# Kernel tuning notes

Hardware: AMD Instinct MI355X
Metric: run time of the kernel (lower is better)

Reference implementation:

```python
import jax, jax.numpy as jnp
import numpy as np

PERTURBATION_SCALE = 0.01

def setup_inputs() -> dict:
    key = jax.random.key(0)
    k1, k2, k3 = jax.random.split(key, 3)
    theta = jax.random.normal(k1, (256, 512), dtype=jnp.float32)
    basis_eval = jax.random.normal(k2, (100000, 512), dtype=jnp.float32)
    noise = jax.random.normal(k3, (256, 512), dtype=jnp.float32)
    return {"theta": theta, "basis_eval": basis_eval, "noise": noise}

def reference(theta, basis_eval, noise):
    # phi: [N, K] functional evaluations
    phi_raw = basis_eval @ theta.T
    phi_perturbed = basis_eval @ (theta + noise * PERTURBATION_SCALE).T
    # sign-crossings between consecutive evaluation points: [N-1, K]
    crossings = (phi_raw[:-1] * phi_raw[1:] < 0).astype(theta.dtype)
    crossings_p = (phi_perturbed[:-1] * phi_perturbed[1:] < 0).astype(theta.dtype)
    persistence = crossings * crossings_p  # [N-1, K]
    # fused pairwise shared-persistence: Gram matrix [K, K]
    gram = persistence.T @ persistence
    K = theta.shape[0]
    iu, ju = jnp.triu_indices(K, k=1)  # row-major i<j == itertools.combinations order
    return gram[iu, ju]  # [K*(K-1)/2]
```

## Files before the change

### kernel.cpp

```cpp
#include <hip/hip_runtime.h>
#include <hip/hip_bf16.h>
#include <stdint.h>

#define KDIM    256
#define NWORDS  1564
#define NW      1563

typedef float  f32x4  __attribute__((ext_vector_type(4)));
typedef __bf16 bf16x8 __attribute__((ext_vector_type(8)));
typedef __bf16 bf16x4 __attribute__((ext_vector_type(4)));

__global__ void build_w(const float* __restrict__ theta,
                        const float* __restrict__ noise,
                        __bf16* __restrict__ Wt) {
    int idx = blockIdx.x * 256 + threadIdx.x;
    int j = idx >> 9;
    int d = idx & 511;
    float v;
    if (j < KDIM) v = theta[j * 512 + d];
    else          v = theta[(j - KDIM) * 512 + d] + 0.01f * noise[(j - KDIM) * 512 + d];
    Wt[((d >> 5) * 512 + j) * 32 + (d & 31)] = (__bf16)v;
}

__global__ void __launch_bounds__(512, 4)
gemm_signs(const float* __restrict__ basis,
           const __bf16* __restrict__ Wt,
           uint64_t* __restrict__ sbits) {
    __shared__ char smem[34816];

    const int tid    = threadIdx.x;
    const int lane   = tid & 63;
    const int wc     = tid >> 6;
    const int lane16 = lane & 15;
    const int lgrp   = lane >> 4;

    const int orig = blockIdx.x;
    const int x    = orig & 7;
    const int bm   = (x < 4 ? x * 196 : 784 + (x - 4) * 195) + (orig >> 3);

    const int rl  = tid >> 3;
    const int oct = tid & 7;
    int r = bm * 64 + rl; if (r > 99999) r = 99999;
    const float* asrc = basis + (size_t)r * 512 + oct * 4;
    const int awofs = rl * 64 + (((oct >> 1) ^ ((rl >> 1) & 3)) << 4) + ((oct & 1) << 3);

    const char* wbase = (const char*)Wt;
    int bfofs[4];
    #pragma unroll
    for (int n = 0; n < 4; ++n)
        bfofs[n] = (wc * 64 + n * 16 + lane16) * 64 + lgrp * 16;

    f32x4  acc[4][4] = {};
    float4 ra[2];
    bf16x8 bf[2][4];

    ra[0] = *(const float4*)(asrc);
    ra[1] = *(const float4*)(asrc + 32);
    #pragma unroll
    for (int n = 0; n < 4; ++n)
        bf[0][n] = *(const bf16x8*)(wbase + bfofs[n]);
    {
        bf16x4 v;
        v[0] = (__bf16)ra[0].x; v[1] = (__bf16)ra[0].y;
        v[2] = (__bf16)ra[0].z; v[3] = (__bf16)ra[0].w;
        *(bf16x4*)(smem + awofs) = v;
    }
    asm volatile("s_waitcnt lgkmcnt(0)" ::: "memory");

    #pragma unroll
    for (int t = 0; t < 16; ++t) {
        if (t < 14) ra[t & 1] = *(const float4*)(asrc + (t + 2) * 32);
        if (t < 15) {
            #pragma unroll
            for (int n = 0; n < 4; ++n)
                bf[(t + 1) & 1][n] =
                    *(const bf16x8*)(wbase + (size_t)(t + 1) * 32768 + bfofs[n]);
        }

        __builtin_amdgcn_s_barrier();

        if (t < 15) {
            bf16x4 v;
            float4 rv = ra[(t + 1) & 1];
            v[0] = (__bf16)rv.x; v[1] = (__bf16)rv.y;
            v[2] = (__bf16)rv.z; v[3] = (__bf16)rv.w;
            *(bf16x4*)(smem + (((t + 1) & 1) << 12) + awofs) = v;
        }

        const char* ab = smem + ((t & 1) << 12);
        #pragma unroll
        for (int mh = 0; mh < 2; ++mh) {
            bf16x8 af[2];
            #pragma unroll
            for (int mi = 0; mi < 2; ++mi) {
                int rr = (mh * 2 + mi) * 16 + lane16;
                af[mi] = *(const bf16x8*)(ab + rr * 64
                           + ((lgrp ^ ((rr >> 1) & 3)) << 4));
            }
            asm volatile("s_waitcnt lgkmcnt(0)" ::: "memory");
            __builtin_amdgcn_sched_barrier(0);
            __builtin_amdgcn_s_setprio(1);
            #pragma unroll
            for (int mi = 0; mi < 2; ++mi)
                #pragma unroll
                for (int n = 0; n < 4; ++n)
                    acc[mh * 2 + mi][n] = __builtin_amdgcn_mfma_f32_16x16x32_bf16(
                        af[mi], bf[t & 1][n], acc[mh * 2 + mi][n], 0, 0, 0);
            __builtin_amdgcn_s_setprio(0);
        }
    }

    __builtin_amdgcn_s_barrier();
    unsigned char* sb = (unsigned char*)smem;
    #pragma unroll
    for (int m = 0; m < 4; ++m) {
        #pragma unroll
        for (int n = 0; n < 4; ++n) {
            int cc = wc * 64 + n * 16 + lane16;
            int rb = m * 16 + lgrp * 4;
            uint32_t pk = 0;
            #pragma unroll
            for (int rg = 0; rg < 4; ++rg)
                pk |= (acc[m][n][rg] < 0.0f ? 1u : 0u) << (8 * rg);
            *(uint32_t*)&sb[cc * 68 + rb] = pk;
        }
    }
    asm volatile("s_waitcnt lgkmcnt(0)" ::: "memory");
    __builtin_amdgcn_s_barrier();

    {
        const unsigned char* src = &sb[tid * 68];
        uint64_t wbits = 0;
        #pragma unroll
        for (int k = 0; k < 16; ++k) {
            uint32_t qv = *(const uint32_t*)&src[4 * k];
            uint32_t p4 = ((qv & 0x01010101u) * 0x10204080u) >> 28;
            wbits |= (uint64_t)p4 << (4 * k);
        }
        sbits[(size_t)bm * 512 + tid] = wbits;
    }
}

__global__ void crossing_masks(const uint64_t* __restrict__ sbits,
                               uint64_t* __restrict__ maskT) {
    const int w = blockIdx.x;
    const int j = threadIdx.x;
    uint64_t s0r = sbits[(size_t)w * 512 + j];
    uint64_t s0p = sbits[(size_t)w * 512 + 256 + j];
    uint64_t s1r = sbits[(size_t)(w + 1) * 512 + j];
    uint64_t s1p = sbits[(size_t)(w + 1) * 512 + 256 + j];
    uint64_t cr = s0r ^ ((s0r >> 1) | (s1r << 63));
    uint64_t cp = s0p ^ ((s0p >> 1) | (s1p << 63));
    uint64_t m = cr & cp;
    if (w == NW - 1) m &= 0x7FFFFFFFull;
    maskT[(size_t)w * 256 + j] = m;
}

__global__ void zero_out(float* __restrict__ out) {
    int i = blockIdx.x * 256 + threadIdx.x;
    if (i < 32640) out[i] = 0.0f;
}

__global__ void pair_popcount(const uint64_t* __restrict__ maskT,
                              float* __restrict__ out) {
    const int i = blockIdx.x;
    const int c = blockIdx.y;
    const int j = threadIdx.x;
    if (j <= i) return;
    int w0 = c * 196;
    int w1 = w0 + 196; if (w1 > NW) w1 = NW;
    uint32_t sum = 0;
    #pragma unroll 4
    for (int w = w0; w < w1; ++w) {
        uint64_t mi = maskT[(size_t)w * 256 + i];
        uint64_t mj = maskT[(size_t)w * 256 + j];
        sum += (uint32_t)__popcll(mi & mj);
    }
    const size_t idx = (size_t)i * (2 * KDIM - i - 1) / 2 + (size_t)(j - i - 1);
    atomicAdd(&out[idx], (float)sum);
}

extern "C" void kernel_launch(void* const* d_in, const int* in_sizes, int n_in,
                              void* d_out, int out_size, void* d_ws, size_t ws_size,
                              hipStream_t stream) {
    const float* theta = (const float*)d_in[0];
    const float* basis = (const float*)d_in[1];
    const float* noise = (const float*)d_in[2];
    float* out = (float*)d_out;

    char* ws = (char*)d_ws;
    __bf16*   Wt    = (__bf16*)ws;
    uint64_t* sbits = (uint64_t*)(ws + 524288);
    uint64_t* maskT = (uint64_t*)(ws + 524288 + (size_t)NWORDS * 512 * 8);

    hipLaunchKernelGGL(build_w,        dim3(1024),    dim3(256), 0, stream, theta, noise, Wt);
    hipLaunchKernelGGL(gemm_signs,     dim3(NWORDS),  dim3(512), 0, stream, basis, Wt, sbits);
    hipLaunchKernelGGL(crossing_masks, dim3(NW),      dim3(256), 0, stream, sbits, maskT);
    hipLaunchKernelGGL(zero_out,       dim3(128),     dim3(256), 0, stream, out);
    hipLaunchKernelGGL(pair_popcount,  dim3(KDIM, 8), dim3(256), 0, stream, maskT, out);
}
```

Baseline: 122.5 us.

## Stage A tiles in 128-wide K chunks to cut barriers in GEMM loop

The A-operand staging in gemm_signs is restructured to load 128 K-elements per row per stage into a larger double-buffered LDS region with XOR swizzling over 16 slots. This drops block barriers from one per 32-K step to one per 128-K step and loads all four A fragments before issuing 16 MFMAs. It also removes the explicit per-half lgkmcnt wait. Launch bounds drop to 2 blocks per CU, which permits more registers for the larger prefetch state but risks lower occupancy.

```diff
diff --git a/kernel.cpp b/kernel.cpp
--- a/kernel.cpp
+++ b/kernel.cpp
@@ -8,7 +8,6 @@
 
 typedef float  f32x4  __attribute__((ext_vector_type(4)));
 typedef __bf16 bf16x8 __attribute__((ext_vector_type(8)));
-typedef __bf16 bf16x4 __attribute__((ext_vector_type(4)));
 
 __global__ void build_w(const float* __restrict__ theta,
                         const float* __restrict__ noise,
@@ -22,7 +21,7 @@
     Wt[((d >> 5) * 512 + j) * 32 + (d & 31)] = (__bf16)v;
 }
 
-__global__ void __launch_bounds__(512, 4)
+__global__ void __launch_bounds__(512, 2)
 gemm_signs(const float* __restrict__ basis,
            const __bf16* __restrict__ Wt,
            uint64_t* __restrict__ sbits) {
@@ -41,8 +40,8 @@
     const int rl  = tid >> 3;
     const int oct = tid & 7;
     int r = bm * 64 + rl; if (r > 99999) r = 99999;
-    const float* asrc = basis + (size_t)r * 512 + oct * 4;
-    const int awofs = rl * 64 + (((oct >> 1) ^ ((rl >> 1) & 3)) << 4) + ((oct & 1) << 3);
+    const float* ag = basis + (size_t)r * 512 + oct * 16;
+    const int gsz = rl & 15;
 
     const char* wbase = (const char*)Wt;
     int bfofs[4];
@@ -51,62 +50,70 @@
         bfofs[n] = (wc * 64 + n * 16 + lane16) * 64 + lgrp * 16;
 
     f32x4  acc[4][4] = {};
-    float4 ra[2];
-    bf16x8 bf[2][4];
-
-    ra[0] = *(const float4*)(asrc);
-    ra[1] = *(const float4*)(asrc + 32);
-    #pragma unroll
-    for (int n = 0; n < 4; ++n)
-        bf[0][n] = *(const bf16x8*)(wbase + bfofs[n]);
-    {
-        bf16x4 v;
-        v[0] = (__bf16)ra[0].x; v[1] = (__bf16)ra[0].y;
-        v[2] = (__bf16)ra[0].z; v[3] = (__bf16)ra[0].w;
-        *(bf16x4*)(smem + awofs) = v;
-    }
+    float4 ra[4];
+    bf16x8 bfr[2][4];
+
+    auto write_A = [&](int q) {
+        char* wb = smem + (q << 14);
+        #pragma unroll
+        for (int u = 0; u < 2; ++u) {
+            bf16x8 w;
+            w[0] = (__bf16)ra[2*u].x;   w[1] = (__bf16)ra[2*u].y;
+            w[2] = (__bf16)ra[2*u].z;   w[3] = (__bf16)ra[2*u].w;
+            w[4] = (__bf16)ra[2*u+1].x; w[5] = (__bf16)ra[2*u+1].y;
+            w[6] = (__bf16)ra[2*u+1].z; w[7] = (__bf16)ra[2*u+1].w;
+            *(bf16x8*)(wb + rl * 256 + (((2*oct + u) ^ gsz) << 4)) = w;
+        }
+    };
+
+    #pragma unroll
+    for (int u = 0; u < 4; ++u) ra[u] = *(const float4*)(ag + u * 4);
+    #pragma unroll
+    for (int n = 0; n < 4; ++n) bfr[0][n] = *(const bf16x8*)(wbase + bfofs[n]);
+    write_A(0);
+    #pragma unroll
+    for (int u = 0; u < 4; ++u) ra[u] = *(const float4*)(ag + 128 + u * 4);
     asm volatile("s_waitcnt lgkmcnt(0)" ::: "memory");
-
-    #pragma unroll
-    for (int t = 0; t < 16; ++t) {
-        if (t < 14) ra[t & 1] = *(const float4*)(asrc + (t + 2) * 32);
-        if (t < 15) {
+    __builtin_amdgcn_s_barrier();
+
+    #pragma unroll
+    for (int s = 0; s < 4; ++s) {
+        const char* ab = smem + ((s & 1) << 14);
+        #pragma unroll
+        for (int ti = 0; ti < 4; ++ti) {
+            const int t = s * 4 + ti;
+            if (t < 15) {
+                #pragma unroll
+                for (int n = 0; n < 4; ++n)
+                    bfr[(t + 1) & 1][n] =
+                        *(const bf16x8*)(wbase + (size_t)(t + 1) * 32768 + bfofs[n]);
+            }
+            bf16x8 af[4];
             #pragma unroll
-            for (int n = 0; n < 4; ++n)
-                bf[(t + 1) & 1][n] =
-                    *(const bf16x8*)(wbase + (size_t)(t + 1) * 32768 + bfofs[n]);
-        }
-
-        __builtin_amdgcn_s_barrier();
-
-        if (t < 15) {
-            bf16x4 v;
-            float4 rv = ra[(t + 1) & 1];
-            v[0] = (__bf16)rv.x; v[1] = (__bf16)rv.y;
-            v[2] = (__bf16)rv.z; v[3] = (__bf16)rv.w;
-            *(bf16x4*)(smem + (((t + 1) & 1) << 12) + awofs) = v;
-        }
-
-        const char* ab = smem + ((t & 1) << 12);
-        #pragma unroll
-        for (int mh = 0; mh < 2; ++mh) {
-            bf16x8 af[2];
-            #pragma unroll
-            for (int mi = 0; mi < 2; ++mi) {
-                int rr = (mh * 2 + mi) * 16 + lane16;
-                af[mi] = *(const bf16x8*)(ab + rr * 64
-                           + ((lgrp ^ ((rr >> 1) & 3)) << 4));
+            for (int m = 0; m < 4; ++m) {
+                int rr = m * 16 + lane16;
+                af[m] = *(const bf16x8*)(ab + rr * 256
+                           + (((ti * 4 + lgrp) ^ (rr & 15)) << 4));
             }
-            asm volatile("s_waitcnt lgkmcnt(0)" ::: "memory");
             __builtin_amdgcn_sched_barrier(0);
             __builtin_amdgcn_s_setprio(1);
             #pragma unroll
-            for (int mi = 0; mi < 2; ++mi)
+            for (int m = 0; m < 4; ++m)
                 #pragma unroll
                 for (int n = 0; n < 4; ++n)
-                    acc[mh * 2 + mi][n] = __builtin_amdgcn_mfma_f32_16x16x32_bf16(
-                        af[mi], bf[t & 1][n], acc[mh * 2 + mi][n], 0, 0, 0);
+                    acc[m][n] = __builtin_amdgcn_mfma_f32_16x16x32_bf16(
+                        af[m], bfr[t & 1][n], acc[m][n], 0, 0, 0);
             __builtin_amdgcn_s_setprio(0);
+        }
+        if (s < 3) {
+            write_A((s + 1) & 1);
+            if (s < 2) {
+                #pragma unroll
+                for (int u = 0; u < 4; ++u)
+                    ra[u] = *(const float4*)(ag + (s + 2) * 128 + u * 4);
+            }
+            asm volatile("s_waitcnt lgkmcnt(0)" ::: "memory");
+            __builtin_amdgcn_s_barrier();
         }
     }
 
```

Result: slower. 139.6 us (+14.0%).

## Warp-specialize GEMM into producer wave loading A and consumer MFMA waves

Applied to the files above, without the earlier changes.

Splits the sign GEMM block into 8 consumer waves doing MFMA and 2 producer waves that load basis rows, convert them to bf16 and fill a 4-slot LDS ring. Handoff uses workgroup-scope atomic ready/done counters instead of block-wide barriers each k-step. The aim is to overlap global loads with MFMA work and drop per-iteration barriers. In exchange, spin-wait polling adds overhead, and the larger block plus launch bounds may reduce occupancy and raise register pressure.

```diff
diff --git a/kernel.cpp b/kernel.cpp
--- a/kernel.cpp
+++ b/kernel.cpp
@@ -22,114 +22,152 @@
     Wt[((d >> 5) * 512 + j) * 32 + (d & 31)] = (__bf16)v;
 }
 
-__global__ void __launch_bounds__(512, 4)
-gemm_signs(const float* __restrict__ basis,
-           const __bf16* __restrict__ Wt,
-           uint64_t* __restrict__ sbits) {
-    __shared__ char smem[34816];
+__global__ void __launch_bounds__(640)
+gemm_signs_pc(const float* __restrict__ basis,
+              const __bf16* __restrict__ Wt,
+              uint64_t* __restrict__ sbits) {
+    __shared__ char smem[34848];
 
     const int tid    = threadIdx.x;
     const int lane   = tid & 63;
-    const int wc     = tid >> 6;
+    const int wave   = tid >> 6;
     const int lane16 = lane & 15;
     const int lgrp   = lane >> 4;
+
+    unsigned* ready     = (unsigned*)(smem + 34816);
+    unsigned* cons_done = (unsigned*)(smem + 34816 + 16);
+    if (tid < 8) ((unsigned*)(smem + 34816))[tid] = 0;
+    __syncthreads();
 
     const int orig = blockIdx.x;
     const int x    = orig & 7;
     const int bm   = (x < 4 ? x * 196 : 784 + (x - 4) * 195) + (orig >> 3);
 
-    const int rl  = tid >> 3;
-    const int oct = tid & 7;
-    int r = bm * 64 + rl; if (r > 99999) r = 99999;
-    const float* asrc = basis + (size_t)r * 512 + oct * 4;
-    const int awofs = rl * 64 + (((oct >> 1) ^ ((rl >> 1) & 3)) << 4) + ((oct & 1) << 3);
-
-    const char* wbase = (const char*)Wt;
-    int bfofs[4];
-    #pragma unroll
-    for (int n = 0; n < 4; ++n)
-        bfofs[n] = (wc * 64 + n * 16 + lane16) * 64 + lgrp * 16;
-
-    f32x4  acc[4][4] = {};
-    float4 ra[2];
-    bf16x8 bf[2][4];
-
-    ra[0] = *(const float4*)(asrc);
-    ra[1] = *(const float4*)(asrc + 32);
-    #pragma unroll
-    for (int n = 0; n < 4; ++n)
-        bf[0][n] = *(const bf16x8*)(wbase + bfofs[n]);
-    {
-        bf16x4 v;
-        v[0] = (__bf16)ra[0].x; v[1] = (__bf16)ra[0].y;
-        v[2] = (__bf16)ra[0].z; v[3] = (__bf16)ra[0].w;
-        *(bf16x4*)(smem + awofs) = v;
-    }
-    asm volatile("s_waitcnt lgkmcnt(0)" ::: "memory");
-
-    #pragma unroll
-    for (int t = 0; t < 16; ++t) {
-        if (t < 14) ra[t & 1] = *(const float4*)(asrc + (t + 2) * 32);
-        if (t < 15) {
-            #pragma unroll
-            for (int n = 0; n < 4; ++n)
-                bf[(t + 1) & 1][n] =
-                    *(const bf16x8*)(wbase + (size_t)(t + 1) * 32768 + bfofs[n]);
-        }
-
-        __builtin_amdgcn_s_barrier();
-
-        if (t < 15) {
-            bf16x4 v;
-            float4 rv = ra[(t + 1) & 1];
-            v[0] = (__bf16)rv.x; v[1] = (__bf16)rv.y;
-            v[2] = (__bf16)rv.z; v[3] = (__bf16)rv.w;
-            *(bf16x4*)(smem + (((t + 1) & 1) << 12) + awofs) = v;
-        }
-
-        const char* ab = smem + ((t & 1) << 12);
-        #pragma unroll
-        for (int mh = 0; mh < 2; ++mh) {
-            bf16x8 af[2];
-            #pragma unroll
-            for (int mi = 0; mi < 2; ++mi) {
-                int rr = (mh * 2 + mi) * 16 + lane16;
-                af[mi] = *(const bf16x8*)(ab + rr * 64
+    char* ring = smem;
+
+    if (wave < 8) {
+        const int wc = wave;
+        const char* wbase = (const char*)Wt;
+        int bfofs[4];
+        #pragma unroll
+        for (int n = 0; n < 4; ++n)
+            bfofs[n] = (wc * 64 + n * 16 + lane16) * 64 + lgrp * 16;
+
+        f32x4  acc[4][4] = {};
+        bf16x8 bf[2][4];
+        #pragma unroll
+        for (int n = 0; n < 4; ++n)
+            bf[0][n] = *(const bf16x8*)(wbase + bfofs[n]);
+
+        #pragma unroll
+        for (int t = 0; t < 16; ++t) {
+            if (t < 15) {
+                #pragma unroll
+                for (int n = 0; n < 4; ++n)
+                    bf[(t + 1) & 1][n] =
+                        *(const bf16x8*)(wbase + (size_t)(t + 1) * 32768 + bfofs[n]);
+            }
+            const int slot = t & 3;
+            const unsigned need = 2u * (unsigned)((t >> 2) + 1);
+            while (__hip_atomic_load(&ready[slot], __ATOMIC_ACQUIRE,
+                                     __HIP_MEMORY_SCOPE_WORKGROUP) < need)
+                __builtin_amdgcn_s_sleep(1);
+
+            const char* ab = ring + slot * 4096;
+            bf16x8 af[4];
+            #pragma unroll
+            for (int m = 0; m < 4; ++m) {
+                int rr = m * 16 + lane16;
+                af[m] = *(const bf16x8*)(ab + rr * 64
                            + ((lgrp ^ ((rr >> 1) & 3)) << 4));
             }
             asm volatile("s_waitcnt lgkmcnt(0)" ::: "memory");
+            if (lane == 0)
+                __hip_atomic_fetch_add(&cons_done[slot], 1u, __ATOMIC_RELEASE,
+                                       __HIP_MEMORY_SCOPE_WORKGROUP);
             __builtin_amdgcn_sched_barrier(0);
             __builtin_amdgcn_s_setprio(1);
             #pragma unroll
-            for (int mi = 0; mi < 2; ++mi)
+            for (int m = 0; m < 4; ++m)
                 #pragma unroll
                 for (int n = 0; n < 4; ++n)
-                    acc[mh * 2 + mi][n] = __builtin_amdgcn_mfma_f32_16x16x32_bf16(
-                        af[mi], bf[t & 1][n], acc[mh * 2 + mi][n], 0, 0, 0);
+                    acc[m][n] = __builtin_amdgcn_mfma_f32_16x16x32_bf16(
+                        af[m], bf[t & 1][n], acc[m][n], 0, 0, 0);
             __builtin_amdgcn_s_setprio(0);
         }
+
+        __syncthreads();
+        unsigned char* sb = (unsigned char*)smem;
+        #pragma unroll
+        for (int m = 0; m < 4; ++m) {
+            #pragma unroll
+            for (int n = 0; n < 4; ++n) {
+                int cc = wc * 64 + n * 16 + lane16;
+                int rb = m * 16 + lgrp * 4;
+                uint32_t pk = 0;
+                #pragma unroll
+                for (int rg = 0; rg < 4; ++rg)
+                    pk |= (acc[m][n][rg] < 0.0f ? 1u : 0u) << (8 * rg);
+                *(uint32_t*)&sb[cc * 68 + rb] = pk;
+            }
+        }
+        asm volatile("s_waitcnt lgkmcnt(0)" ::: "memory");
+        __syncthreads();
+    } else {
+        const int ptid = tid - 512;
+        const int oct  = ptid & 7;
+        const int p    = ptid >> 3;
+        int rbase[4];
+        #pragma unroll
+        for (int i = 0; i < 4; ++i) {
+            int r = bm * 64 + p + 16 * i;
+            rbase[i] = (r > 99999) ? 99999 : r;
+        }
+        const int aw0 = (p) * 64 + (((oct >> 1) ^ ((p >> 1) & 3)) << 4)
+                        + ((oct & 1) << 3);
+
+        float4 ra[2][4];
+        #pragma unroll
+        for (int i = 0; i < 4; ++i)
+            ra[0][i] = *(const float4*)(basis + (size_t)rbase[i] * 512 + oct * 4);
+
+        #pragma unroll
+        for (int t = 0; t < 16; ++t) {
+            if (t < 15) {
+                #pragma unroll
+                for (int i = 0; i < 4; ++i)
+                    ra[(t + 1) & 1][i] = *(const float4*)
+                        (basis + (size_t)rbase[i] * 512 + (t + 1) * 32 + oct * 4);
+            }
+            const int slot = t & 3;
+            const unsigned r = (unsigned)(t >> 2);
+            if (r > 0) {
+                const unsigned need = 8u * r;
+                while (__hip_atomic_load(&cons_done[slot], __ATOMIC_ACQUIRE,
+                                         __HIP_MEMORY_SCOPE_WORKGROUP) < need)
+                    __builtin_amdgcn_s_sleep(1);
+            }
+            char* wb = ring + slot * 4096;
+            #pragma unroll
+            for (int i = 0; i < 4; ++i) {
+                float4 rv = ra[t & 1][i];
+                bf16x4 v;
+                v[0] = (__bf16)rv.x; v[1] = (__bf16)rv.y;
+                v[2] = (__bf16)rv.z; v[3] = (__bf16)rv.w;
+                *(bf16x4*)(wb + aw0 + 1024 * i) = v;
+            }
+            asm volatile("s_waitcnt lgkmcnt(0)" ::: "memory");
+            if (lane == 0)
+                __hip_atomic_fetch_add(&ready[slot], 1u, __ATOMIC_RELEASE,
+                                       __HIP_MEMORY_SCOPE_WORKGROUP);
+        }
+
+        __syncthreads();
+        __syncthreads();
     }
 
-    __builtin_amdgcn_s_barrier();
-    unsigned char* sb = (unsigned char*)smem;
-    #pragma unroll
-    for (int m = 0; m < 4; ++m) {
-        #pragma unroll
-        for (int n = 0; n < 4; ++n) {
-            int cc = wc * 64 + n * 16 + lane16;
-            int rb = m * 16 + lgrp * 4;
-            uint32_t pk = 0;
-            #pragma unroll
-            for (int rg = 0; rg < 4; ++rg)
-                pk |= (acc[m][n][rg] < 0.0f ? 1u : 0u) << (8 * rg);
-            *(uint32_t*)&sb[cc * 68 + rb] = pk;
-        }
-    }
-    asm volatile("s_waitcnt lgkmcnt(0)" ::: "memory");
-    __builtin_amdgcn_s_barrier();
-
-    {
-        const unsigned char* src = &sb[tid * 68];
+    if (tid < 512) {
+        const unsigned char* src = (const unsigned char*)smem + tid * 68;
         uint64_t wbits = 0;
         #pragma unroll
         for (int k = 0; k < 16; ++k) {
@@ -194,7 +232,7 @@
     uint64_t* maskT = (uint64_t*)(ws + 524288 + (size_t)NWORDS * 512 * 8);
 
     hipLaunchKernelGGL(build_w,        dim3(1024),    dim3(256), 0, stream, theta, noise, Wt);
-    hipLaunchKernelGGL(gemm_signs,     dim3(NWORDS),  dim3(512), 0, stream, basis, Wt, sbits);
+    hipLaunchKernelGGL(gemm_signs_pc,  dim3(NWORDS),  dim3(640), 0, stream, basis, Wt, sbits);
     hipLaunchKernelGGL(crossing_masks, dim3(NW),      dim3(256), 0, stream, sbits, maskT);
     hipLaunchKernelGGL(zero_out,       dim3(128),     dim3(256), 0, stream, out);
     hipLaunchKernelGGL(pair_popcount,  dim3(KDIM, 8), dim3(256), 0, stream, maskT, out);
```

New measurement: 132.8 us. +8.4%, slower.

## Stage whole A tile in LDS upfront instead of per-step double buffering

Applied to the files above, without the earlier changes.

The GEMM kernel now loads the entire 64x512 fp32 basis tile with 16 wide loads per thread, converts it to bf16 and stores it in a 64KB XOR-swizzled LDS buffer before the K loop. This removes the per-iteration barrier and LDS double-buffer writes from the main loop, so the MFMA loop only issues B register loads and LDS reads. The cost is more LDS per block (64KB vs 34KB), which lowers occupancy, plus an exposed upfront global-load latency with no overlap against compute.

```diff
diff --git a/kernel.cpp b/kernel.cpp
--- a/kernel.cpp
+++ b/kernel.cpp
@@ -26,7 +26,7 @@
 gemm_signs(const float* __restrict__ basis,
            const __bf16* __restrict__ Wt,
            uint64_t* __restrict__ sbits) {
-    __shared__ char smem[34816];
+    __shared__ char smem[65536];
 
     const int tid    = threadIdx.x;
     const int lane   = tid & 63;
@@ -38,67 +38,59 @@
     const int x    = orig & 7;
     const int bm   = (x < 4 ? x * 196 : 784 + (x - 4) * 195) + (orig >> 3);
 
-    const int rl  = tid >> 3;
-    const int oct = tid & 7;
-    int r = bm * 64 + rl; if (r > 99999) r = 99999;
-    const float* asrc = basis + (size_t)r * 512 + oct * 4;
-    const int awofs = rl * 64 + (((oct >> 1) ^ ((rl >> 1) & 3)) << 4) + ((oct & 1) << 3);
-
     const char* wbase = (const char*)Wt;
     int bfofs[4];
     #pragma unroll
     for (int n = 0; n < 4; ++n)
         bfofs[n] = (wc * 64 + n * 16 + lane16) * 64 + lgrp * 16;
 
-    f32x4  acc[4][4] = {};
-    float4 ra[2];
     bf16x8 bf[2][4];
-
-    ra[0] = *(const float4*)(asrc);
-    ra[1] = *(const float4*)(asrc + 32);
     #pragma unroll
     for (int n = 0; n < 4; ++n)
         bf[0][n] = *(const bf16x8*)(wbase + bfofs[n]);
+
     {
-        bf16x4 v;
-        v[0] = (__bf16)ra[0].x; v[1] = (__bf16)ra[0].y;
-        v[2] = (__bf16)ra[0].z; v[3] = (__bf16)ra[0].w;
-        *(bf16x4*)(smem + awofs) = v;
+        const int rlo  = tid >> 7;
+        const int cidx = (tid * 4) & 511;
+        const int fg   = tid & 127;
+        const int gsl  = fg >> 1;
+        const int ghl  = (fg & 1) << 3;
+        f32x4 ra[16];
+        #pragma unroll
+        for (int j = 0; j < 16; ++j) {
+            int r = bm * 64 + j * 4 + rlo;
+            if (r > 99999) r = 99999;
+            ra[j] = *(const f32x4*)(basis + (size_t)r * 512 + cidx);
+        }
+        #pragma unroll
+        for (int j = 0; j < 16; ++j) {
+            const int row = j * 4 + rlo;
+            bf16x4 v;
+            v[0] = (__bf16)ra[j][0]; v[1] = (__bf16)ra[j][1];
+            v[2] = (__bf16)ra[j][2]; v[3] = (__bf16)ra[j][3];
+            *(bf16x4*)(smem + row * 1024 + ((gsl ^ row) << 4) + ghl) = v;
+        }
     }
-    asm volatile("s_waitcnt lgkmcnt(0)" ::: "memory");
+    __syncthreads();
 
+    f32x4 acc[4][4] = {};
     #pragma unroll
     for (int t = 0; t < 16; ++t) {
-        if (t < 14) ra[t & 1] = *(const float4*)(asrc + (t + 2) * 32);
         if (t < 15) {
             #pragma unroll
             for (int n = 0; n < 4; ++n)
                 bf[(t + 1) & 1][n] =
                     *(const bf16x8*)(wbase + (size_t)(t + 1) * 32768 + bfofs[n]);
         }
-
-        __builtin_amdgcn_s_barrier();
-
-        if (t < 15) {
-            bf16x4 v;
-            float4 rv = ra[(t + 1) & 1];
-            v[0] = (__bf16)rv.x; v[1] = (__bf16)rv.y;
-            v[2] = (__bf16)rv.z; v[3] = (__bf16)rv.w;
-            *(bf16x4*)(smem + (((t + 1) & 1) << 12) + awofs) = v;
-        }
-
-        const char* ab = smem + ((t & 1) << 12);
         #pragma unroll
         for (int mh = 0; mh < 2; ++mh) {
             bf16x8 af[2];
             #pragma unroll
             for (int mi = 0; mi < 2; ++mi) {
                 int rr = (mh * 2 + mi) * 16 + lane16;
-                af[mi] = *(const bf16x8*)(ab + rr * 64
-                           + ((lgrp ^ ((rr >> 1) & 3)) << 4));
+                af[mi] = *(const bf16x8*)(smem + rr * 1024
+                           + (((t * 4 + lgrp) ^ rr) << 4));
             }
-            asm volatile("s_waitcnt lgkmcnt(0)" ::: "memory");
-            __builtin_amdgcn_sched_barrier(0);
             __builtin_amdgcn_s_setprio(1);
             #pragma unroll
             for (int mi = 0; mi < 2; ++mi)
@@ -110,7 +102,7 @@
         }
     }
 
-    __builtin_amdgcn_s_barrier();
+    __syncthreads();
     unsigned char* sb = (unsigned char*)smem;
     #pragma unroll
     for (int m = 0; m < 4; ++m) {
@@ -125,8 +117,7 @@
             *(uint32_t*)&sb[cc * 68 + rb] = pk;
         }
     }
-    asm volatile("s_waitcnt lgkmcnt(0)" ::: "memory");
-    __builtin_amdgcn_s_barrier();
+    __syncthreads();
 
     {
         const unsigned char* src = &sb[tid * 68];
```

Result: slower. 129.9 us (+6.1%).
